# Optimization experiments

Hardware: AMD Instinct MI355X
Metric: run time of the kernel (lower is better)

## Reference

```python
import jax, jax.numpy as jnp
import numpy as np

# ---- module hyperparameters (from init_kwargs) ----
N_REPL = 4      # n
NUM_FM = 32
D = 2
PRD = 2
K_SZ = 2 * D + 1
ALPHA = 0.1
ETA = 0.1
THETA = 0.1
EPS = 1e-10


def symm_pad(x, p):
    # faithful to torch symm_pad: sequential in-place border reflection
    x = x.at[..., :p, :].set(jnp.flip(x[..., p:2 * p, :], axis=-2))
    x = x.at[..., -p:, :].set(jnp.flip(x[..., -2 * p:-p, :], axis=-2))
    x = x.at[..., :, :p].set(jnp.flip(x[..., :, p:2 * p], axis=-1))
    x = x.at[..., :, -p:].set(jnp.flip(x[..., :, -2 * p:-p], axis=-1))
    return x


def pad_activations(A, prd=PRD, d=D):
    H, W = A.shape[-2], A.shape[-1]
    pz = jnp.zeros(A.shape[:-2] + (prd * d + H, prd * d + W), A.dtype)
    pz = pz.at[..., prd:-prd, prd:-prd].set(A)
    return symm_pad(pz, 2 * prd)


def minmax_on_fm(x):
    # min-max normalize each feature map (last two dims) to [0,1]
    mn = x.min(axis=(-2, -1), keepdims=True)
    mx = x.max(axis=(-2, -1), keepdims=True)
    return (x - mn) / (mx - mn + EPS)


def softmax_on_fm(x):
    sh = x.shape
    return jax.nn.softmax(x.reshape(sh[:-2] + (-1,)), axis=-1).reshape(sh)


def softmax_minmax_scaled(x):
    return softmax_on_fm(minmax_on_fm(x))


def conv2d(x, w):
    # x: (B, Cin, H, W), w: (Cout, Cin, k, k), valid conv
    return jax.lax.conv_general_dilated(
        x, w, window_strides=(1, 1), padding='VALID',
        dimension_numbers=('NCHW', 'OIHW', 'NCHW'))


def setup_inputs() -> dict:
    key = jax.random.key(0)
    kA, kK, kN = jax.random.split(key, 3)
    C = N_REPL * NUM_FM
    A = jax.random.uniform(kA, (16, NUM_FM, 56, 56), jnp.float32)
    # K initialized as softmax_on_fm(rand), matching __init__
    K = softmax_on_fm(jax.random.uniform(kK, (C, C, K_SZ, K_SZ), jnp.float32))
    noise = jax.random.normal(kN, (16, C, 56, 56), jnp.float32)
    return {"A": A, "K": K, "noise": noise}


def reference(A, K, noise):
    B, num_fm, H, W = A.shape
    n, d, prd, k = N_REPL, D, PRD, K_SZ
    C = n * num_fm

    A = symm_pad(A, prd)                              # (B, num_fm, H, W)
    Ab = jnp.tile(A, (1, n, 1, 1))                    # (B, C, H, W)
    Ab = jnp.clip(Ab + ETA * noise, 0.0)
    pA = pad_activations(Ab)                          # (B, C, H+4, W+4)

    # torch does K.transpose_(0,1) in place; K1 is the post-transpose K
    K1 = jnp.swapaxes(K, 0, 1)
    L = conv2d(pA, minmax_on_fm(K1)) / num_fm         # (B, C, H, W)
    L = softmax_minmax_scaled(L)

    # winner-take-all across the n replicas of each feature map
    s = (Ab + L).sum(axis=(-2, -1)).reshape(B, n, num_fm)
    winners = jnp.argmax(jnp.swapaxes(s, 1, 2), axis=-1)          # (B, num_fm)
    fm_idx = num_fm * winners + jnp.arange(num_fm)                # (B, num_fm)
    win_mask = jnp.zeros((B, C), Ab.dtype).at[
        jnp.arange(B)[:, None], fm_idx].set(1.0)                  # 1 at winning channels

    # ---- Hebbian K update: per-offset masked cross-correlation ----
    Am = Ab * win_mask[:, :, None, None]  # zero losing *source* channels
    cols = []
    for x in range(k):
        xo = -d + x
        rows = []
        for y in range(k):
            yo = -d + y
            src = Am[:, :, max(0, xo):H + min(xo, 0), max(0, yo):W + min(yo, 0)]
            tgt = Ab[:, :, max(0, -xo):H + min(-xo, 0), max(0, -yo):W + min(-yo, 0)]
            rows.append(jnp.einsum('bchw,bahw->ca', src, tgt) / (C * B))
        cols.append(jnp.stack(rows, axis=-1))        # (C, C, k) over y
    K_change = jnp.stack(cols, axis=-2)              # (C, C, k, k) indexed [c,a,x,y]

    K2 = (1.0 - ALPHA) * K1 + ALPHA * minmax_on_fm(K_change)

    # ---- second lateral pass with losing channels zeroed ----
    A2 = Ab * win_mask[:, :, None, None]
    # torch zeroes only diagonal filters K[c,c] of losing c per sample; since the
    # corresponding input channels of A2 are exactly zero, a single shared-weight
    # conv is mathematically identical.
    L2 = conv2d(pad_activations(A2), minmax_on_fm(jnp.swapaxes(K2, 0, 1))) / num_fm

    gather = lambda X: jnp.take_along_axis(X, fm_idx[:, :, None, None], axis=1)
    O = gather(A2) + THETA * gather(L2)              # (B, num_fm, H, W)
    return O
```

## Files before the change

kernel.cpp:

```cpp
#include <hip/hip_runtime.h>


typedef __attribute__((ext_vector_type(8))) short short8;
typedef __attribute__((ext_vector_type(4))) float floatx4;

#define EPSF 1e-10f

__device__ __forceinline__ int map60(int r) {
  return r < 4 ? 5 - r : (r < 56 ? r - 2 : 109 - r);
}
__device__ __forceinline__ unsigned short f2bf(float x) {
  unsigned int u = __float_as_uint(x);
  u += 0x7fff + ((u >> 16) & 1);
  return (unsigned short)(u >> 16);
}
__device__ __forceinline__ float bf2f(unsigned int h) {
  return __uint_as_float((h & 0xffffu) << 16);
}

__global__ __launch_bounds__(256) void k1_build(const float* __restrict__ A,
                                                const float* __restrict__ noise,
                                                unsigned short* __restrict__ Abf,
                                                float* __restrict__ s) {
  int bc = blockIdx.x;
  int b = bc >> 7, c = bc & 127;
  int fm = c & 31;
  const float* Abase = A + (size_t)(b * 32 + fm) * 3136;
  const float* nz = noise + (size_t)bc * 3136;
  unsigned short* outb = Abf + 128 + (size_t)bc * 3840;
  float local = 0.f;
  for (int q = threadIdx.x; q < 960; q += 256) {
    int r = q >> 4, qc = q & 15, col0 = qc << 2;
    int h = r - 2;
    float v0, v1, v2, v3;
    if (r < 2 || r > 57 || qc == 15) {
      v0 = v1 = v2 = v3 = 0.f;
    } else if (r >= 4 && r <= 55 && qc >= 1 && qc <= 13) {
      int w0 = col0 - 2;
      const float* ap = Abase + h * 56 + w0;
      const float* np = nz + h * 56 + w0;
      float2 a0 = *reinterpret_cast<const float2*>(ap);
      float2 a1 = *reinterpret_cast<const float2*>(ap + 2);
      float2 n0 = *reinterpret_cast<const float2*>(np);
      float2 n1 = *reinterpret_cast<const float2*>(np + 2);
      v0 = fmaxf(a0.x + 0.1f * n0.x, 0.f);
      v1 = fmaxf(a0.y + 0.1f * n0.y, 0.f);
      v2 = fmaxf(a1.x + 0.1f * n1.x, 0.f);
      v3 = fmaxf(a1.y + 0.1f * n1.y, 0.f);
    } else {
      float vv[4];
      int hh = h < 2 ? 3 - h : (h >= 54 ? 107 - h : h);
#pragma unroll
      for (int j = 0; j < 4; j++) {
        int w = col0 + j - 2;
        float v = 0.f;
        if ((unsigned)w < 56u) {
          int ww = w < 2 ? 3 - w : (w >= 54 ? 107 - w : w);
          v = fmaxf(Abase[hh * 56 + ww] + 0.1f * nz[h * 56 + w], 0.f);
        }
        vv[j] = v;
      }
      v0 = vv[0]; v1 = vv[1]; v2 = vv[2]; v3 = vv[3];
    }
    local += v0 + v1 + v2 + v3;
    uint2 w;
    w.x = (unsigned)f2bf(v0) | ((unsigned)f2bf(v1) << 16);
    w.y = (unsigned)f2bf(v2) | ((unsigned)f2bf(v3) << 16);
    *reinterpret_cast<uint2*>(outb + r * 64 + col0) = w;
  }
  int lane = threadIdx.x & 63, wid = threadIdx.x >> 6;
  float v = local;
  for (int off = 32; off; off >>= 1) v += __shfl_down(v, off, 64);
  __shared__ float red[4];
  if (lane == 0) red[wid] = v;
  __syncthreads();
  if (threadIdx.x == 0) s[bc] = red[0] + red[1] + red[2] + red[3];
}

__global__ __launch_bounds__(512) void k2_winners(const float* __restrict__ s,
                                                  int* __restrict__ fm_idx,
                                                  int* __restrict__ cmask,
                                                  unsigned short* __restrict__ Abf) {
  int t = threadIdx.x;
  {
    int b = t >> 5, f = t & 31;
    float best = s[b * 128 + f];
    int bn = 0;
    for (int n = 1; n < 4; n++) {
      float v = s[b * 128 + n * 32 + f];
      if (v > best) { best = v; bn = n; }
    }
    fm_idx[t] = bn * 32 + f;
  }
  if (t < 128) Abf[t] = 0;
  if (t >= 384) Abf[128 + 7864320 + (t - 384)] = 0;
  __syncthreads();
  if (t < 128) {
    int m = 0;
    for (int b = 0; b < 16; b++)
      if (fm_idx[b * 32 + (t & 31)] == t) m |= (1 << b);
    cmask[t] = m;
  }
}

__global__ __launch_bounds__(256) void k2c_shift(const unsigned short* __restrict__ Abf,
                                                 const int* __restrict__ fm_idx,
                                                 unsigned short* __restrict__ Sb) {
  int bx = blockIdx.x;
  int g = bx & 31, b = bx >> 5;
  int c = fm_idx[b * 32 + g];
  const unsigned short* src = Abf + 128 + (size_t)(b * 128 + c) * 3840;
  unsigned short* dbase = Sb + (size_t)b * 5 * 122880 + g * 3840;
  for (int q = threadIdx.x; q < 480; q += 256) {
    int p0 = q * 8;
    uint4 M = *reinterpret_cast<const uint4*>(src + p0);
    unsigned L = (q == 0) ? 0u : *reinterpret_cast<const unsigned*>(src + p0 - 2);
    unsigned R = (q == 479) ? 0u : *reinterpret_cast<const unsigned*>(src + p0 + 8);
    unsigned u0 = L, u1 = M.x, u2 = M.y, u3 = M.z, u4 = M.w, u5 = R;
    uint4 o;
    o.x = u0; o.y = u1; o.z = u2; o.w = u3;
    *reinterpret_cast<uint4*>(dbase + 4 * 122880 + p0) = o;
    o.x = __builtin_amdgcn_alignbit(u1, u0, 16);
    o.y = __builtin_amdgcn_alignbit(u2, u1, 16);
    o.z = __builtin_amdgcn_alignbit(u3, u2, 16);
    o.w = __builtin_amdgcn_alignbit(u4, u3, 16);
    *reinterpret_cast<uint4*>(dbase + 3 * 122880 + p0) = o;
    o.x = u1; o.y = u2; o.z = u3; o.w = u4;
    *reinterpret_cast<uint4*>(dbase + 2 * 122880 + p0) = o;
    o.x = __builtin_amdgcn_alignbit(u2, u1, 16);
    o.y = __builtin_amdgcn_alignbit(u3, u2, 16);
    o.z = __builtin_amdgcn_alignbit(u4, u3, 16);
    o.w = __builtin_amdgcn_alignbit(u5, u4, 16);
    *reinterpret_cast<uint4*>(dbase + 1 * 122880 + p0) = o;
    o.x = u2; o.y = u3; o.z = u4; o.w = u5;
    *reinterpret_cast<uint4*>(dbase + p0) = o;
  }
}

__global__ __launch_bounds__(256) void k2t_transpose(const unsigned short* __restrict__ Abf,
                                                     const int* __restrict__ fm_idx,
                                                     unsigned short* __restrict__ T) {
  __shared__ int win[32];
  int b = blockIdx.x / 15, chunk = blockIdx.x % 15;
  if (threadIdx.x < 32) win[threadIdx.x] = fm_idx[b * 32 + threadIdx.x];
  __syncthreads();
  int p = chunk * 256 + threadIdx.x;
  int r = p >> 6, s2 = p & 63;
  int mr = map60(r) + 2;
  int ms = (s2 < 60) ? map60(s2) + 2 : -1;
  unsigned int out[16];
#pragma unroll
  for (int gp = 0; gp < 16; gp++) {
    unsigned short v0 = 0, v1 = 0;
    if (ms >= 0) {
      v0 = Abf[128 + ((size_t)(b * 128) + win[2 * gp]) * 3840 + mr * 64 + ms];
      v1 = Abf[128 + ((size_t)(b * 128) + win[2 * gp + 1]) * 3840 + mr * 64 + ms];
    }
    out[gp] = (unsigned)v0 | ((unsigned)v1 << 16);
  }
  uint4* dst = reinterpret_cast<uint4*>(T + (size_t)b * 122880 + (size_t)p * 32);
#pragma unroll
  for (int q = 0; q < 4; q++) {
    uint4 u;
    u.x = out[4 * q]; u.y = out[4 * q + 1]; u.z = out[4 * q + 2]; u.w = out[4 * q + 3];
    dst[q] = u;
  }
}

__global__ __launch_bounds__(256) void k3_mfma(const unsigned short* __restrict__ Sb,
                                               const unsigned short* __restrict__ Abf,
                                               float* __restrict__ Kc_b) {
  int bx = blockIdx.x;
  int nt = bx & 7, mt = (bx >> 3) & 1, kh = (bx >> 4) & 1, b = bx >> 5;
  int wave = threadIdx.x >> 6, lane = threadIdx.x & 63;
  int al = lane & 15, quad = lane >> 4;
  int g0 = mt * 16, a0 = nt * 16;
  int k0 = kh * 1920 + wave * 480;
  floatx4 acc[5][5];
#pragma unroll
  for (int i = 0; i < 5; i++)
#pragma unroll
    for (int j = 0; j < 5; j++) acc[i][j] = (floatx4){0.f, 0.f, 0.f, 0.f};
  const short8* pA[5];
#pragma unroll
  for (int di = 0; di < 5; di++)
    pA[di] = reinterpret_cast<const short8*>(
        Sb + (size_t)(b * 5 + di) * 122880 + (size_t)(g0 + al) * 3840 + k0 + quad * 8);
  const short8* pB = reinterpret_cast<const short8*>(
      Abf + 128 + (size_t)(b * 128 + a0 + al) * 3840 + k0 + quad * 8) - 16;
  for (int ks = 0; ks < 15; ks++) {
    short8 afr[5], bfr[5];
#pragma unroll
    for (int d = 0; d < 5; d++) afr[d] = pA[d][0];
#pragma unroll
    for (int d = 0; d < 5; d++) bfr[d] = pB[d * 8];
#pragma unroll
    for (int di = 0; di < 5; di++)
#pragma unroll
      for (int dj = 0; dj < 5; dj++)
        acc[di][dj] =
            __builtin_amdgcn_mfma_f32_16x16x32_bf16(afr[di], bfr[dj], acc[di][dj], 0, 0, 0);
#pragma unroll
    for (int d = 0; d < 5; d++) pA[d] += 4;
    pB += 4;
  }
  __shared__ float red[6400];
  float* myrow = red + lane * 100;
  if (wave == 0) {
#pragma unroll
    for (int di = 0; di < 5; di++)
#pragma unroll
      for (int dj = 0; dj < 5; dj++)
#pragma unroll
        for (int r = 0; r < 4; r++) myrow[(di * 5 + dj) * 4 + r] = acc[di][dj][r];
  }
  __syncthreads();
#pragma unroll
  for (int w = 1; w < 4; w++) {
    if (wave == w) {
#pragma unroll
      for (int di = 0; di < 5; di++)
#pragma unroll
        for (int dj = 0; dj < 5; dj++)
#pragma unroll
          for (int r = 0; r < 4; r++) myrow[(di * 5 + dj) * 4 + r] += acc[di][dj][r];
    }
    __syncthreads();
  }
  if (wave == 0) {
    int slot = b * 2 + kh;
#pragma unroll
    for (int di = 0; di < 5; di++)
#pragma unroll
      for (int dj = 0; dj < 5; dj++) {
        int t_out = 24 - (dj * 5 + di);
#pragma unroll
        for (int r = 0; r < 4; r++) {
          int g = g0 + quad * 4 + r;
          Kc_b[(((size_t)slot * 32 + g) * 128 + (a0 + al)) * 25 + t_out] =
              myrow[(di * 5 + dj) * 4 + r] * (1.0f / 2048.0f);
        }
      }
  }
}

__global__ __launch_bounds__(256) void k4_weights(const float* __restrict__ Kc_b,
                                                  const float* __restrict__ K,
                                                  const int* __restrict__ cmask,
                                                  unsigned short* __restrict__ W2g) {
  int gid = blockIdx.x * 256 + threadIdx.x;
  int o = gid >> 7, i = gid & 127;
  int mi = cmask[i], mo = cmask[o];
  float kc[25];
#pragma unroll
  for (int t = 0; t < 25; t++) kc[t] = 0.f;
  for (int slot = 0; slot < 32; slot++) {
    if ((mi >> (slot >> 1)) & 1) {
      const float* p = Kc_b + (((size_t)slot * 32 + (i & 31)) * 128 + o) * 25;
#pragma unroll
      for (int t = 0; t < 25; t++) kc[t] += p[t];
    }
  }
  float mn = 1e30f, mx = -1e30f;
#pragma unroll
  for (int t = 0; t < 25; t++) { mn = fminf(mn, kc[t]); mx = fmaxf(mx, kc[t]); }
  float d1 = mx - mn + EPSF;
  const float* kp = K + ((size_t)o * 128 + i) * 25;
  float k2[25], mn2 = 1e30f, mx2 = -1e30f;
#pragma unroll
  for (int t = 0; t < 25; t++) {
    k2[t] = 0.9f * kp[t] + 0.1f * ((kc[t] - mn) / d1);
    mn2 = fminf(mn2, k2[t]);
    mx2 = fmaxf(mx2, k2[t]);
  }
  float d2 = mx2 - mn2 + EPSF;
  unsigned short wb[25];
#pragma unroll
  for (int t = 0; t < 25; t++) wb[t] = f2bf((k2[t] - mn2) / d2);
  int mw = mo & mi;
  int f = o & 31, g = i & 31;
  while (mw) {
    int b = __ffs(mw) - 1;
    mw &= mw - 1;
    unsigned short* dst = W2g + ((size_t)(b * 25) * 32 + f) * 32 + g;
#pragma unroll
    for (int t = 0; t < 25; t++) dst[(size_t)t * 1024] = wb[t];
  }
}

__global__ __launch_bounds__(64) void k5_mfma(const unsigned short* __restrict__ W2g,
                                              const unsigned short* __restrict__ T,
                                              const unsigned short* __restrict__ Abf,
                                              const int* __restrict__ fm_idx,
                                              float* __restrict__ O) {
  int bx = blockIdx.x;
  int rg = bx % 14;
  int mtb = bx / 14;
  int mt = mtb & 1, b = mtb >> 1;
  int lane = threadIdx.x, al = lane & 15, quad = lane >> 4;
  int fm = mt * 16 + al;
  short8 afr[25];
#pragma unroll
  for (int t = 0; t < 25; t++)
    afr[t] = *reinterpret_cast<const short8*>(
        W2g + ((size_t)((b * 25 + t) * 32 + fm) << 5) + quad * 8);
  int orow[4];
#pragma unroll
  for (int r = 0; r < 4; r++) orow[r] = fm_idx[b * 32 + mt * 16 + quad * 4 + r];
  const unsigned short* Tb = T + (size_t)b * 122880;
  for (int rr = 0; rr < 4; rr++) {
    int row = 2 + rg * 4 + rr;
    for (int pair = 0; pair < 2; pair++) {
      int px0 = row * 64 + pair * 32 + al;
      floatx4 acca = (floatx4){0.f, 0.f, 0.f, 0.f};
      floatx4 accb = (floatx4){0.f, 0.f, 0.f, 0.f};
#pragma unroll
      for (int t = 0; t < 25; t++) {
        int off = (t / 5 - 2) * 64 + (t % 5) - 2;
        const short8* pb = reinterpret_cast<const short8*>(
            Tb + (ptrdiff_t)(px0 + off) * 32 + quad * 8);
        short8 b0 = pb[0];
        short8 b1 = pb[64];
        acca = __builtin_amdgcn_mfma_f32_16x16x32_bf16(afr[t], b0, acca, 0, 0, 0);
        accb = __builtin_amdgcn_mfma_f32_16x16x32_bf16(afr[t], b1, accb, 0, 0, 0);
      }
      int h = row - 2;
#pragma unroll
      for (int half = 0; half < 2; half++) {
        floatx4 acc = half ? accb : acca;
        int cc = pair * 32 + half * 16 + al;
        if (cc >= 2 && cc < 58) {
          int w = cc - 2;
          int px = row * 64 + cc;
#pragma unroll
          for (int r = 0; r < 4; r++) {
            int f = mt * 16 + quad * 4 + r;
            float base = bf2f(Abf[128 + (size_t)(b * 128 + orow[r]) * 3840 + px]);
            O[(size_t)(b * 32 + f) * 3136 + h * 56 + w] = base + acc[r] * (0.1f / 32.0f);
          }
        }
      }
    }
  }
}

extern "C" void kernel_launch(void* const* d_in, const int* in_sizes, int n_in,
                              void* d_out, int out_size, void* d_ws, size_t ws_size,
                              hipStream_t stream) {
  const float* A = (const float*)d_in[0];
  const float* K = (const float*)d_in[1];
  const float* noise = (const float*)d_in[2];
  float* O = (float*)d_out;

  float* ws = (float*)d_ws;
  unsigned short* Abf = (unsigned short*)ws;
  float* s = ws + 3932288;
  int* fm_idx = (int*)(ws + 3934336);
  int* cmask = (int*)(ws + 3934848);
  float* Kc_b = ws + 3934976;
  unsigned short* T = (unsigned short*)(ws + 7211776);
  unsigned short* Sb = (unsigned short*)(ws + 8194816);
  unsigned short* W2g = (unsigned short*)(ws + 8194816);

  k1_build<<<2048, 256, 0, stream>>>(A, noise, Abf, s);
  k2_winners<<<1, 512, 0, stream>>>(s, fm_idx, cmask, Abf);
  k2c_shift<<<512, 256, 0, stream>>>(Abf, fm_idx, Sb);
  k2t_transpose<<<240, 256, 0, stream>>>(Abf, fm_idx, T);
  k3_mfma<<<512, 256, 0, stream>>>(Sb, Abf, Kc_b);
  k4_weights<<<64, 256, 0, stream>>>(Kc_b, K, cmask, W2g);
  k5_mfma<<<448, 64, 0, stream>>>(W2g, T, Abf, fm_idx, O);
}
```

Measured before the change: 188.3 us.

## Drop shifted-copy kernel; build column-shifted operands in registers via alignbit

Removes the k2c_shift kernel, which wrote five column-shifted bf16 copies of the winning channels to global memory. k3_mfma now gathers winner rows through fm_idx and builds the shifted B-fragments on the fly from overlapping loads combined with alignbit. Block indexing is reordered so batch is the fastest-varying index, and the Abf guard padding grows from 128 to 256 elements so the wider halo reads stay in bounds. This saves a kernel launch and a large write-then-read of the shifted copies, at the cost of extra unaligned loads and ALU work inside the MFMA loop.

```diff
diff --git a/kernel.cpp b/kernel.cpp
--- a/kernel.cpp
+++ b/kernel.cpp
@@ -16,6 +16,11 @@
 }
 __device__ __forceinline__ float bf2f(unsigned int h) {
   return __uint_as_float((h & 0xffffu) << 16);
+}
+__device__ __forceinline__ short8 u4_to_s8(uint4 v) {
+  union { uint4 u; short8 s; } cv;
+  cv.u = v;
+  return cv.s;
 }
 
 __global__ __launch_bounds__(256) void k1_build(const float* __restrict__ A,
@@ -27,7 +32,7 @@
   int fm = c & 31;
   const float* Abase = A + (size_t)(b * 32 + fm) * 3136;
   const float* nz = noise + (size_t)bc * 3136;
-  unsigned short* outb = Abf + 128 + (size_t)bc * 3840;
+  unsigned short* outb = Abf + 256 + (size_t)bc * 3840;
   float local = 0.f;
   for (int q = threadIdx.x; q < 960; q += 256) {
     int r = q >> 4, qc = q & 15, col0 = qc << 2;
@@ -92,48 +97,14 @@
     }
     fm_idx[t] = bn * 32 + f;
   }
-  if (t < 128) Abf[t] = 0;
-  if (t >= 384) Abf[128 + 7864320 + (t - 384)] = 0;
+  if (t < 256) Abf[t] = 0;
+  if (t >= 256) Abf[256 + 7864320 + (t - 256)] = 0;
   __syncthreads();
   if (t < 128) {
     int m = 0;
     for (int b = 0; b < 16; b++)
       if (fm_idx[b * 32 + (t & 31)] == t) m |= (1 << b);
     cmask[t] = m;
-  }
-}
-
-__global__ __launch_bounds__(256) void k2c_shift(const unsigned short* __restrict__ Abf,
-                                                 const int* __restrict__ fm_idx,
-                                                 unsigned short* __restrict__ Sb) {
-  int bx = blockIdx.x;
-  int g = bx & 31, b = bx >> 5;
-  int c = fm_idx[b * 32 + g];
-  const unsigned short* src = Abf + 128 + (size_t)(b * 128 + c) * 3840;
-  unsigned short* dbase = Sb + (size_t)b * 5 * 122880 + g * 3840;
-  for (int q = threadIdx.x; q < 480; q += 256) {
-    int p0 = q * 8;
-    uint4 M = *reinterpret_cast<const uint4*>(src + p0);
-    unsigned L = (q == 0) ? 0u : *reinterpret_cast<const unsigned*>(src + p0 - 2);
-    unsigned R = (q == 479) ? 0u : *reinterpret_cast<const unsigned*>(src + p0 + 8);
-    unsigned u0 = L, u1 = M.x, u2 = M.y, u3 = M.z, u4 = M.w, u5 = R;
-    uint4 o;
-    o.x = u0; o.y = u1; o.z = u2; o.w = u3;
-    *reinterpret_cast<uint4*>(dbase + 4 * 122880 + p0) = o;
-    o.x = __builtin_amdgcn_alignbit(u1, u0, 16);
-    o.y = __builtin_amdgcn_alignbit(u2, u1, 16);
-    o.z = __builtin_amdgcn_alignbit(u3, u2, 16);
-    o.w = __builtin_amdgcn_alignbit(u4, u3, 16);
-    *reinterpret_cast<uint4*>(dbase + 3 * 122880 + p0) = o;
-    o.x = u1; o.y = u2; o.z = u3; o.w = u4;
-    *reinterpret_cast<uint4*>(dbase + 2 * 122880 + p0) = o;
-    o.x = __builtin_amdgcn_alignbit(u2, u1, 16);
-    o.y = __builtin_amdgcn_alignbit(u3, u2, 16);
-    o.z = __builtin_amdgcn_alignbit(u4, u3, 16);
-    o.w = __builtin_amdgcn_alignbit(u5, u4, 16);
-    *reinterpret_cast<uint4*>(dbase + 1 * 122880 + p0) = o;
-    o.x = u2; o.y = u3; o.z = u4; o.w = u5;
-    *reinterpret_cast<uint4*>(dbase + p0) = o;
   }
 }
 
@@ -153,8 +124,8 @@
   for (int gp = 0; gp < 16; gp++) {
     unsigned short v0 = 0, v1 = 0;
     if (ms >= 0) {
-      v0 = Abf[128 + ((size_t)(b * 128) + win[2 * gp]) * 3840 + mr * 64 + ms];
-      v1 = Abf[128 + ((size_t)(b * 128) + win[2 * gp + 1]) * 3840 + mr * 64 + ms];
+      v0 = Abf[256 + ((size_t)(b * 128) + win[2 * gp]) * 3840 + mr * 64 + ms];
+      v1 = Abf[256 + ((size_t)(b * 128) + win[2 * gp + 1]) * 3840 + mr * 64 + ms];
     }
     out[gp] = (unsigned)v0 | ((unsigned)v1 << 16);
   }
@@ -167,11 +138,13 @@
   }
 }
 
-__global__ __launch_bounds__(256) void k3_mfma(const unsigned short* __restrict__ Sb,
-                                               const unsigned short* __restrict__ Abf,
+__global__ __launch_bounds__(256) void k3_mfma(const unsigned short* __restrict__ Abf,
+                                               const int* __restrict__ fm_idx,
                                                float* __restrict__ Kc_b) {
   int bx = blockIdx.x;
-  int nt = bx & 7, mt = (bx >> 3) & 1, kh = (bx >> 4) & 1, b = bx >> 5;
+  int b = bx & 15;
+  int rr = bx >> 4;
+  int kh = rr & 1, mt = (rr >> 1) & 1, nt = rr >> 2;
   int wave = threadIdx.x >> 6, lane = threadIdx.x & 63;
   int al = lane & 15, quad = lane >> 4;
   int g0 = mt * 16, a0 = nt * 16;
@@ -181,28 +154,35 @@
   for (int i = 0; i < 5; i++)
 #pragma unroll
     for (int j = 0; j < 5; j++) acc[i][j] = (floatx4){0.f, 0.f, 0.f, 0.f};
-  const short8* pA[5];
-#pragma unroll
-  for (int di = 0; di < 5; di++)
-    pA[di] = reinterpret_cast<const short8*>(
-        Sb + (size_t)(b * 5 + di) * 122880 + (size_t)(g0 + al) * 3840 + k0 + quad * 8);
-  const short8* pB = reinterpret_cast<const short8*>(
-      Abf + 128 + (size_t)(b * 128 + a0 + al) * 3840 + k0 + quad * 8) - 16;
+  int c = fm_idx[b * 32 + g0 + al];
+  const unsigned short* pA = Abf + 256 + (size_t)(b * 128 + c) * 3840 + k0 + quad * 8;
+  const unsigned short* pB = Abf + 256 + (size_t)(b * 128 + a0 + al) * 3840 + k0 + quad * 8;
   for (int ks = 0; ks < 15; ks++) {
-    short8 afr[5], bfr[5];
-#pragma unroll
-    for (int d = 0; d < 5; d++) afr[d] = pA[d][0];
-#pragma unroll
-    for (int d = 0; d < 5; d++) bfr[d] = pB[d * 8];
-#pragma unroll
-    for (int di = 0; di < 5; di++)
-#pragma unroll
-      for (int dj = 0; dj < 5; dj++)
-        acc[di][dj] =
-            __builtin_amdgcn_mfma_f32_16x16x32_bf16(afr[di], bfr[dj], acc[di][dj], 0, 0, 0);
-#pragma unroll
-    for (int d = 0; d < 5; d++) pA[d] += 4;
-    pB += 4;
+    short8 afr = *reinterpret_cast<const short8*>(pA);
+#pragma unroll
+    for (int dj = 0; dj < 5; dj++) {
+      const unsigned short* bb = pB + 64 * (dj - 2);
+      uint2 L = *reinterpret_cast<const uint2*>(bb - 4);
+      uint4 M = *reinterpret_cast<const uint4*>(bb);
+      uint2 R = *reinterpret_cast<const uint2*>(bb + 8);
+      unsigned ab0 = __builtin_amdgcn_alignbit(M.x, L.y, 16);
+      unsigned ab1 = __builtin_amdgcn_alignbit(M.y, M.x, 16);
+      unsigned ab2 = __builtin_amdgcn_alignbit(M.z, M.y, 16);
+      unsigned ab3 = __builtin_amdgcn_alignbit(M.w, M.z, 16);
+      unsigned ab4 = __builtin_amdgcn_alignbit(R.x, M.w, 16);
+      acc[0][dj] = __builtin_amdgcn_mfma_f32_16x16x32_bf16(
+          afr, u4_to_s8((uint4){L.y, M.x, M.y, M.z}), acc[0][dj], 0, 0, 0);
+      acc[1][dj] = __builtin_amdgcn_mfma_f32_16x16x32_bf16(
+          afr, u4_to_s8((uint4){ab0, ab1, ab2, ab3}), acc[1][dj], 0, 0, 0);
+      acc[2][dj] = __builtin_amdgcn_mfma_f32_16x16x32_bf16(
+          afr, u4_to_s8((uint4){M.x, M.y, M.z, M.w}), acc[2][dj], 0, 0, 0);
+      acc[3][dj] = __builtin_amdgcn_mfma_f32_16x16x32_bf16(
+          afr, u4_to_s8((uint4){ab1, ab2, ab3, ab4}), acc[3][dj], 0, 0, 0);
+      acc[4][dj] = __builtin_amdgcn_mfma_f32_16x16x32_bf16(
+          afr, u4_to_s8((uint4){M.y, M.z, M.w, R.x}), acc[4][dj], 0, 0, 0);
+    }
+    pA += 32;
+    pB += 32;
   }
   __shared__ float red[6400];
   float* myrow = red + lane * 100;
@@ -335,7 +315,7 @@
 #pragma unroll
           for (int r = 0; r < 4; r++) {
             int f = mt * 16 + quad * 4 + r;
-            float base = bf2f(Abf[128 + (size_t)(b * 128 + orow[r]) * 3840 + px]);
+            float base = bf2f(Abf[256 + (size_t)(b * 128 + orow[r]) * 3840 + px]);
             O[(size_t)(b * 32 + f) * 3136 + h * 56 + w] = base + acc[r] * (0.1f / 32.0f);
           }
         }
@@ -354,19 +334,17 @@
 
   float* ws = (float*)d_ws;
   unsigned short* Abf = (unsigned short*)ws;
-  float* s = ws + 3932288;
-  int* fm_idx = (int*)(ws + 3934336);
-  int* cmask = (int*)(ws + 3934848);
-  float* Kc_b = ws + 3934976;
-  unsigned short* T = (unsigned short*)(ws + 7211776);
-  unsigned short* Sb = (unsigned short*)(ws + 8194816);
-  unsigned short* W2g = (unsigned short*)(ws + 8194816);
+  float* s = ws + 3932416;
+  int* fm_idx = (int*)(ws + 3934464);
+  int* cmask = (int*)(ws + 3934976);
+  float* Kc_b = ws + 3935104;
+  unsigned short* T = (unsigned short*)(ws + 7211904);
+  unsigned short* W2g = (unsigned short*)(ws + 8194944);
 
   k1_build<<<2048, 256, 0, stream>>>(A, noise, Abf, s);
   k2_winners<<<1, 512, 0, stream>>>(s, fm_idx, cmask, Abf);
-  k2c_shift<<<512, 256, 0, stream>>>(Abf, fm_idx, Sb);
   k2t_transpose<<<240, 256, 0, stream>>>(Abf, fm_idx, T);
-  k3_mfma<<<512, 256, 0, stream>>>(Sb, Abf, Kc_b);
+  k3_mfma<<<512, 256, 0, stream>>>(Abf, fm_idx, Kc_b);
   k4_weights<<<64, 256, 0, stream>>>(Kc_b, K, cmask, W2g);
   k5_mfma<<<448, 64, 0, stream>>>(W2g, T, Abf, fm_idx, O);
 }
```

Result: no change. 186.5 us (-1.0%).
